# Optimization experiments

Hardware: AMD Instinct MI355X
Metric: run time of the kernel (lower is better)

## Reference

```python
import jax, jax.numpy as jnp
import numpy as np

# ReRAM crossbar constants (from init_kwargs)
GMAX = 0.000333
GMIN = 3.33e-07
DELTA_G = GMAX - GMIN
VDD = 3.3
N_LVL_V = 256
DELTA_V = VDD / (N_LVL_V - 1)
CRXB_COL, CRXB_ROW, CRXB_SIZE = 16, 16, 64
BATCH = 4096


def setup_inputs() -> dict:
    key = jax.random.key(0)
    k1, k2 = jax.random.split(key)
    inputs = jax.random.normal(k1, (BATCH, 1, CRXB_ROW, CRXB_SIZE, 1), dtype=jnp.float32)
    weight = jax.random.normal(k2, (CRXB_COL, CRXB_ROW, CRXB_SIZE, CRXB_SIZE), dtype=jnp.float32)
    nchout_index = jnp.arange(CRXB_COL * CRXB_SIZE, dtype=jnp.int64)
    return {"inputs": inputs, "weight": weight, "nchout_index": nchout_index}


def reference(inputs, weight, nchout_index):
    # DAC: scale digital input to voltage
    input_crxb = inputs * DELTA_V                      # [N,1,row,S,1]
    # w2g: map signed weight to positive/negative conductance crossbars
    g_pos = GMIN + jax.nn.relu(weight) * DELTA_G       # [col,row,S,S]
    g_neg = GMIN + jax.nn.relu(-weight) * DELTA_G
    # split pos/neg crossbar matmuls (broadcast over batch), fused subtract
    out = jnp.matmul(g_pos, input_crxb) - jnp.matmul(g_neg, input_crxb)  # [N,col,row,S,1]
    out = jnp.swapaxes(out, 2, 3)                      # [N,col,S,row,1]
    n = out.shape[0]
    out = out.reshape(n, CRXB_COL * CRXB_SIZE, CRXB_ROW, 1)
    out = jnp.take(out, nchout_index, axis=1)          # output channel select
    return jnp.squeeze(out, axis=-1)                   # [N, col*S, row]
```

## Files before the change

### kernel.cpp

```cpp
#include <hip/hip_runtime.h>
#include <hip/hip_bf16.h>
#include <stdint.h>


using bf16x8 = __attribute__((ext_vector_type(8))) short;
using f32x4  = __attribute__((ext_vector_type(4))) float;
using f32x2  = __attribute__((ext_vector_type(2))) float;

#define NPT 16
#define NIT 16
#define PITCH_B 2064
#define OPITCH_DW 514
#define BUFB 33024
#define LDS_BYTES (2*BUFB)

#define BARRIER() asm volatile("s_waitcnt lgkmcnt(0)\n\ts_barrier" ::: "memory")

__device__ inline bf16x8 cvt8v(float4 a, float4 b) {
  union { bf16x8 v; __hip_bfloat162 h[4]; } r;
  r.h[0] = __float22bfloat162_rn(float2{a.x, a.y});
  r.h[1] = __float22bfloat162_rn(float2{a.z, a.w});
  r.h[2] = __float22bfloat162_rn(float2{b.x, b.y});
  r.h[3] = __float22bfloat162_rn(float2{b.z, b.w});
  return r.v;
}

__global__ __launch_bounds__(512, 4)
void crxb_kernel(const float* __restrict__ X, const float* __restrict__ W,
                 float* __restrict__ out) {
  extern __shared__ char smem[];
  const int t   = threadIdx.x;
  const int bid = blockIdx.x;
  const int ngrp = ((bid & 7) << 1) | ((bid >> 3) & 1);
  const int mt   = bid >> 4;
  const int c  = mt >> 1;
  const int i0 = (mt & 1) << 5;
  const int m0 = mt << 5;

  const int wid = t >> 6;
  const int l   = t & 63;
  const int lr  = l & 15;
  const int lk  = l >> 4;
  const int r0w = wid << 1;

  const float S = (float)((0.000333 - 3.33e-07) * (3.3 / 255.0));

  bf16x8 A[2][2][2];
  #pragma unroll
  for (int rr = 0; rr < 2; ++rr)
    #pragma unroll
    for (int ks = 0; ks < 2; ++ks)
      #pragma unroll
      for (int a = 0; a < 2; ++a) {
        const float* gw = W + (((size_t)(c * 16 + r0w + rr) * 64) + (i0 + a * 16 + lr)) * 64
                            + ks * 32 + lk * 8;
        float4 wa = *(const float4*)gw;
        float4 wb = *(const float4*)(gw + 4);
        wa.x *= S; wa.y *= S; wa.z *= S; wa.w *= S;
        wb.x *= S; wb.y *= S; wb.z *= S; wb.w *= S;
        A[rr][ks][a] = cvt8v(wa, wb);
      }

  {
    #pragma unroll
    for (int p = 0; p < 4; ++p) {
      int u = p * 512 + t;
      int n = u >> 7, r = (u >> 3) & 15, k8 = u & 7;
      const float* gx = X + (((size_t)(ngrp * 256 + n) * 16) + r) * 64 + k8 * 8;
      *(bf16x8*)(smem + (size_t)n * PITCH_B + r * 128 + k8 * 16) =
          cvt8v(*(const float4*)gx, *(const float4*)(gx + 4));
    }
  }
  BARRIER();

  int cur = 0;
  for (int it = 0; it < NIT; ++it) {
    char* bufc = smem + cur * BUFB;
    char* bufn = smem + (cur ^ 1) * BUFB;
    const int n0 = ngrp * 256 + it * NPT;

    float4 xp[8];
    if (it + 1 < NIT) {
      #pragma unroll
      for (int p = 0; p < 4; ++p) {
        int u = p * 512 + t;
        int n = u >> 7, r = (u >> 3) & 15, k8 = u & 7;
        const float* gx = X + (((size_t)(n0 + NPT + n) * 16) + r) * 64 + k8 * 8;
        xp[2 * p]     = *(const float4*)gx;
        xp[2 * p + 1] = *(const float4*)(gx + 4);
      }
    }

    f32x4 acc[2][2];
    #pragma unroll
    for (int rr = 0; rr < 2; ++rr)
      #pragma unroll
      for (int a = 0; a < 2; ++a) acc[rr][a] = (f32x4){0.f, 0.f, 0.f, 0.f};

    #pragma unroll
    for (int rr = 0; rr < 2; ++rr) {
      const int r = r0w + rr;
      #pragma unroll
      for (int ks = 0; ks < 2; ++ks) {
        bf16x8 Bf = *(const bf16x8*)(bufc + (size_t)lr * PITCH_B + r * 128 + ks * 64 + lk * 16);
        acc[rr][0] = __builtin_amdgcn_mfma_f32_16x16x32_bf16(A[rr][ks][0], Bf, acc[rr][0], 0, 0, 0);
        acc[rr][1] = __builtin_amdgcn_mfma_f32_16x16x32_bf16(A[rr][ks][1], Bf, acc[rr][1], 0, 0, 0);
      }
    }
    BARRIER();

    {
      float* Od = (float*)bufc;
      #pragma unroll
      for (int a = 0; a < 2; ++a)
        #pragma unroll
        for (int reg = 0; reg < 4; ++reg) {
          f32x2 v = {acc[0][a][reg], acc[1][a][reg]};
          const int mm = a * 16 + lk * 4 + reg;
          *(f32x2*)(Od + (size_t)lr * OPITCH_DW + mm * 16 + r0w) = v;
        }
    }
    BARRIER();

    {
      const int n  = t >> 5;
      const int j0 = t & 31;
      const float* Or = (const float*)bufc + (size_t)n * OPITCH_DW;
      float* gout = out + ((size_t)(n0 + n)) * 16384 + (size_t)m0 * 16;
      #pragma unroll
      for (int q = 0; q < 4; ++q) {
        const int u = (q * 32 + j0) * 4;
        f32x2 lo = *(const f32x2*)(Or + u);
        f32x2 hi = *(const f32x2*)(Or + u + 2);
        f32x4 v = {lo[0], lo[1], hi[0], hi[1]};
        __builtin_nontemporal_store(v, (f32x4*)(gout + u));
      }
    }

    if (it + 1 < NIT) {
      #pragma unroll
      for (int p = 0; p < 4; ++p) {
        int u = p * 512 + t;
        int n = u >> 7, r = (u >> 3) & 15, k8 = u & 7;
        *(bf16x8*)(bufn + (size_t)n * PITCH_B + r * 128 + k8 * 16) = cvt8v(xp[2 * p], xp[2 * p + 1]);
      }
    }
    BARRIER();
    cur ^= 1;
  }
}

extern "C" void kernel_launch(void* const* d_in, const int* in_sizes, int n_in,
                              void* d_out, int out_size, void* d_ws, size_t ws_size,
                              hipStream_t stream) {
  const float* X = (const float*)d_in[0];
  const float* W = (const float*)d_in[1];
  float* out = (float*)d_out;
  (void)in_sizes; (void)n_in; (void)d_ws; (void)ws_size; (void)out_size;

  (void)hipFuncSetAttribute(reinterpret_cast<const void*>(crxb_kernel),
                            hipFuncAttributeMaxDynamicSharedMemorySize, LDS_BYTES);

  crxb_kernel<<<dim3(512), dim3(512), LDS_BYTES, stream>>>(X, W, out);
}
```

Before: 59.90 us.

## Split into bf16 pre-swizzle kernel and LDS-light main kernel

A new pre-pass converts the inputs to bf16 and writes them into a workspace already laid out in MFMA fragment order. The main kernel then reads B fragments straight from global memory, with no LDS staging or double-buffering. This lowers LDS use enough to double occupancy and the grid size. The cost is an extra kernel launch and an extra write and read of the converted input. The old single-kernel path stays as a fallback when the workspace is too small.

```diff
diff --git a/kernel.cpp b/kernel.cpp
--- a/kernel.cpp
+++ b/kernel.cpp
@@ -7,12 +7,8 @@
 using f32x4  = __attribute__((ext_vector_type(4))) float;
 using f32x2  = __attribute__((ext_vector_type(2))) float;
 
-#define NPT 16
-#define NIT 16
-#define PITCH_B 2064
 #define OPITCH_DW 514
-#define BUFB 33024
-#define LDS_BYTES (2*BUFB)
+#define OLDS_BYTES (16 * OPITCH_DW * 4)
 
 #define BARRIER() asm volatile("s_waitcnt lgkmcnt(0)\n\ts_barrier" ::: "memory")
 
@@ -24,6 +20,112 @@
   r.h[3] = __float22bfloat162_rn(float2{b.z, b.w});
   return r.v;
 }
+
+__global__ __launch_bounds__(512, 8)
+void crxb_pre(const float* __restrict__ X, ushort* __restrict__ Xt) {
+  const int g  = blockIdx.x * 512 + threadIdx.x;
+  const int n  = g >> 7;
+  const int r  = (g >> 3) & 15;
+  const int j0 = g & 7;
+  const float* gx = X + (((size_t)n * 16) + r) * 64 + j0 * 8;
+  bf16x8 v = cvt8v(*(const float4*)gx, *(const float4*)(gx + 4));
+  const int ks = j0 >> 2, lk = j0 & 3;
+  const size_t fi = ((((size_t)(n >> 4) * 16 + r) * 2 + ks) * 4 + lk) * 16 + (n & 15);
+  *(bf16x8*)(Xt + fi * 8) = v;
+}
+
+__global__ __launch_bounds__(512, 8)
+void crxb_main(const ushort* __restrict__ Xt, const float* __restrict__ W,
+               float* __restrict__ out) {
+  __shared__ float O[16 * OPITCH_DW];
+
+  const int t   = threadIdx.x;
+  const int bid = blockIdx.x;
+  const int xcd = bid & 7;
+  const int ng  = xcd * 4 + ((bid >> 3) & 3);
+  const int mt  = bid >> 5;
+  const int c  = mt >> 1;
+  const int i0 = (mt & 1) << 5;
+  const int m0 = mt << 5;
+
+  const int wid = t >> 6;
+  const int l   = t & 63;
+  const int lr  = l & 15;
+  const int lk  = l >> 4;
+  const int r0w = wid << 1;
+
+  const float S = (float)((0.000333 - 3.33e-07) * (3.3 / 255.0));
+
+  bf16x8 A[2][2][2];
+  #pragma unroll
+  for (int rr = 0; rr < 2; ++rr)
+    #pragma unroll
+    for (int ks = 0; ks < 2; ++ks)
+      #pragma unroll
+      for (int a = 0; a < 2; ++a) {
+        const float* gw = W + (((size_t)(c * 16 + r0w + rr) * 64) + (i0 + a * 16 + lr)) * 64
+                            + ks * 32 + lk * 8;
+        float4 wa = *(const float4*)gw;
+        float4 wb = *(const float4*)(gw + 4);
+        wa.x *= S; wa.y *= S; wa.z *= S; wa.w *= S;
+        wb.x *= S; wb.y *= S; wb.z *= S; wb.w *= S;
+        A[rr][ks][a] = cvt8v(wa, wb);
+      }
+
+  for (int it = 0; it < 8; ++it) {
+    const int tg = ng * 8 + it;
+    const int n0 = tg * 16;
+
+    f32x4 acc[2][2];
+    #pragma unroll
+    for (int rr = 0; rr < 2; ++rr)
+      #pragma unroll
+      for (int a = 0; a < 2; ++a) acc[rr][a] = (f32x4){0.f, 0.f, 0.f, 0.f};
+
+    #pragma unroll
+    for (int rr = 0; rr < 2; ++rr) {
+      const int r = r0w + rr;
+      #pragma unroll
+      for (int ks = 0; ks < 2; ++ks) {
+        bf16x8 Bf = *(const bf16x8*)(Xt + ((((size_t)tg * 16 + r) * 2 + ks) * 64 + l) * 8);
+        acc[rr][0] = __builtin_amdgcn_mfma_f32_16x16x32_bf16(A[rr][ks][0], Bf, acc[rr][0], 0, 0, 0);
+        acc[rr][1] = __builtin_amdgcn_mfma_f32_16x16x32_bf16(A[rr][ks][1], Bf, acc[rr][1], 0, 0, 0);
+      }
+    }
+    BARRIER();
+
+    #pragma unroll
+    for (int a = 0; a < 2; ++a)
+      #pragma unroll
+      for (int reg = 0; reg < 4; ++reg) {
+        f32x2 v = {acc[0][a][reg], acc[1][a][reg]};
+        const int mm = a * 16 + lk * 4 + reg;
+        *(f32x2*)(O + (size_t)lr * OPITCH_DW + mm * 16 + r0w) = v;
+      }
+    BARRIER();
+
+    {
+      const int n  = t >> 5;
+      const int j0 = t & 31;
+      const float* Or = O + (size_t)n * OPITCH_DW;
+      float* gout = out + ((size_t)(n0 + n)) * 16384 + (size_t)m0 * 16;
+      #pragma unroll
+      for (int q = 0; q < 4; ++q) {
+        const int u = (q * 32 + j0) * 4;
+        f32x2 lo = *(const f32x2*)(Or + u);
+        f32x2 hi = *(const f32x2*)(Or + u + 2);
+        f32x4 v = {lo[0], lo[1], hi[0], hi[1]};
+        __builtin_nontemporal_store(v, (f32x4*)(gout + u));
+      }
+    }
+  }
+}
+
+#define NPT 16
+#define NIT 16
+#define PITCH_B 2064
+#define BUFB 33024
+#define LDS_BYTES (2*BUFB)
 
 __global__ __launch_bounds__(512, 4)
 void crxb_kernel(const float* __restrict__ X, const float* __restrict__ W,
@@ -36,13 +138,11 @@
   const int c  = mt >> 1;
   const int i0 = (mt & 1) << 5;
   const int m0 = mt << 5;
-
   const int wid = t >> 6;
   const int l   = t & 63;
   const int lr  = l & 15;
   const int lk  = l >> 4;
   const int r0w = wid << 1;
-
   const float S = (float)((0.000333 - 3.33e-07) * (3.3 / 255.0));
 
   bf16x8 A[2][2][2];
@@ -156,10 +256,16 @@
   const float* X = (const float*)d_in[0];
   const float* W = (const float*)d_in[1];
   float* out = (float*)d_out;
-  (void)in_sizes; (void)n_in; (void)d_ws; (void)ws_size; (void)out_size;
-
-  (void)hipFuncSetAttribute(reinterpret_cast<const void*>(crxb_kernel),
-                            hipFuncAttributeMaxDynamicSharedMemorySize, LDS_BYTES);
-
-  crxb_kernel<<<dim3(512), dim3(512), LDS_BYTES, stream>>>(X, W, out);
-}
+  (void)in_sizes; (void)n_in; (void)out_size;
+
+  const size_t XT_BYTES = (size_t)4096 * 16 * 64 * 2;
+  if (ws_size >= XT_BYTES) {
+    ushort* Xt = (ushort*)d_ws;
+    crxb_pre <<<dim3(1024), dim3(512), 0, stream>>>(X, Xt);
+    crxb_main<<<dim3(1024), dim3(512), 0, stream>>>(Xt, W, out);
+  } else {
+    (void)hipFuncSetAttribute(reinterpret_cast<const void*>(crxb_kernel),
+                              hipFuncAttributeMaxDynamicSharedMemorySize, LDS_BYTES);
+    crxb_kernel<<<dim3(512), dim3(512), LDS_BYTES, stream>>>(X, W, out);
+  }
+}
```

After: 75.49 us. 26.0% more time.
